# Kernel tuning notes

Hardware: AMD Instinct MI355X
Metric: run time of the kernel (lower is better)

Reference implementation:

```python
import jax, jax.numpy as jnp
import numpy as np

B = 8192
D_S, D_W, D_P, D_E, D_C, D_Z = 1024, 1024, 512, 1024, 512, 512
H_P = 2 * D_P          # particle hidden_dim default
RANK = D_W // 4        # low-rank A factor
EPS = 1e-5             # torch LayerNorm default eps


def _ln(x, g, b):
    m = jnp.mean(x, axis=-1, keepdims=True)
    v = jnp.var(x, axis=-1, keepdims=True)
    return (x - m) * jax.lax.rsqrt(v + EPS) * g + b


def setup_inputs() -> dict:
    key = jax.random.key(0)
    ks = iter(jax.random.split(key, 48))
    def randn(shape, scale=1.0):
        return jax.random.normal(next(ks), shape, dtype=jnp.float32) * scale
    def lin(dout, din):  # torch Linear: W [out,in], b [out]
        s = 1.0 / np.sqrt(din)
        return randn((dout, din), s), randn((dout,), s)
    inp = {}
    inp["s_prev"] = randn((B, D_S))
    inp["w_prev"] = randn((B, D_W))
    inp["p_prev"] = randn((B, D_P))
    inp["e_t"] = randn((B, D_E))
    inp["c_t"] = randn((B, D_C))
    d_in = D_S + D_E + D_C
    # fusion_net: Linear -> LN -> ReLU -> Linear
    inp["fw1"], inp["fb1"] = lin(2 * D_Z, d_in)
    inp["fln_g"] = jnp.ones((2 * D_Z,), jnp.float32)
    inp["fln_b"] = jnp.zeros((2 * D_Z,), jnp.float32)
    inp["fw2"], inp["fb2"] = lin(D_Z, 2 * D_Z)
    # wave subsystem
    inp["A_diag"] = jnp.zeros((D_W,), jnp.float32)
    inp["A_U"] = randn((D_W, RANK), 0.01)
    inp["A_V"] = randn((D_W, RANK), 0.01)
    inp["amod_w"], inp["amod_b"] = lin(D_W, D_C)
    inp["bnet_w"], inp["bnet_b"] = lin(D_W, D_C + D_Z)
    # particle subsystem phi
    inp["pw1"], inp["pb1"] = lin(H_P, D_P + D_Z + D_C)
    inp["pln_g"] = jnp.ones((H_P,), jnp.float32)
    inp["pln_b"] = jnp.zeros((H_P,), jnp.float32)
    inp["pw2"], inp["pb2"] = lin(H_P // 2, H_P)
    inp["pw3"], inp["pb3"] = lin(D_P, H_P // 2)
    # gate + mixing projections + output norm
    inp["gw"], inp["gb"] = lin(D_S, d_in)
    inp["uw"] = randn((D_S, D_W), 1.0 / np.sqrt(D_W))
    inp["up"] = randn((D_S, D_P), 1.0 / np.sqrt(D_P))
    inp["oln_g"] = jnp.ones((D_S,), jnp.float32)
    inp["oln_b"] = jnp.zeros((D_S,), jnp.float32)
    return inp


def reference(s_prev, w_prev, p_prev, e_t, c_t,
              fw1, fb1, fln_g, fln_b, fw2, fb2,
              A_diag, A_U, A_V, amod_w, amod_b, bnet_w, bnet_b,
              pw1, pb1, pln_g, pln_b, pw2, pb2, pw3, pb3,
              gw, gb, uw, up, oln_g, oln_b):
    # fusion: z_t = Linear(ReLU(LN(Linear([s||e||c]))))
    fin = jnp.concatenate([s_prev, e_t, c_t], axis=-1)      # [B, d_s+d_e+d_c]
    h = jax.nn.relu(_ln(fin @ fw1.T + fb1, fln_g, fln_b))
    z_t = h @ fw2.T + fb2                                   # [B, d_z]
    # wave: A = (diag(tanh(A_diag)*0.9) + A_U A_V^T) * mod[None,:]
    # so (A w)[b,i] = sum_j A_base[i,j] * (mod*w)[b,j] -> (mod*w) @ A_base^T
    A_base = jnp.diag(jnp.tanh(A_diag) * 0.9) + A_U @ A_V.T  # [d_w, d_w]
    mod = jnp.tanh(c_t @ amod_w.T + amod_b)                  # [B, d_w]
    w_linear = (mod * w_prev) @ A_base.T
    b_in = jnp.concatenate([c_t, z_t], axis=-1)
    w_t = w_linear + b_in @ bnet_w.T + bnet_b                # [B, d_w]
    # particle: p_t = p_prev + tanh(MLP([p||z||c]))
    pin = jnp.concatenate([p_prev, z_t, c_t], axis=-1)
    h1 = jax.nn.relu(_ln(pin @ pw1.T + pb1, pln_g, pln_b))
    h2 = jax.nn.relu(h1 @ pw2.T + pb2)
    p_t = p_prev + jnp.tanh(h2 @ pw3.T + pb3)                # [B, d_p]
    # gated mixing
    g_t = jax.nn.sigmoid(fin @ gw.T + gb)                    # [B, d_s]
    s_t = s_prev + g_t * (p_t @ up.T) + (1.0 - g_t) * (w_t @ uw.T)
    s_t = _ln(s_t, oln_g, oln_b)
    return (s_t, w_t, p_t)
```

## Files before the change

### kernel.cpp

```cpp
#include <hip/hip_runtime.h>
#include <math.h>

typedef unsigned short u16;
typedef __attribute__((ext_vector_type(8))) short short8;
typedef __attribute__((ext_vector_type(4))) float f32x4;

#define AS1C(p) ((const __attribute__((address_space(1))) void*)(p))
#define AS3(p)  ((__attribute__((address_space(3))) void*)(p))

static __device__ __forceinline__ float b2f(u16 h) {
    union { unsigned u; float f; } c; c.u = ((unsigned)h) << 16; return c.f;
}
static __device__ __forceinline__ u16 f2b(float f) {
    union { float f; unsigned u; } c; c.f = f;
    unsigned r = c.u + 0x7FFFu + ((c.u >> 16) & 1u);
    return (u16)(r >> 16);
}

#define EP_NONE     0
#define EP_RELU     1
#define EP_SIGMOID  2
#define EP_TANH_MUL 3
#define EP_TANH_ADD 4
#define EP_DIAG     5

struct GDesc {
    const u16* A;
    const u16* W;
    const float* bias;
    const float* auxf;
    u16* outb;
    float* outf;
    int lda, ldd, N, K, ep, nbm;
};

struct GArgs { GDesc d0, d1, d2; int s1, s2; };

__global__ __launch_bounds__(512, 2)
void gemm_8p(GArgs ga)
{
    __shared__ __align__(16) u16 LDS[65536];

    const int bid = (int)blockIdx.x;
    GDesc dd = (bid < ga.s1) ? ga.d0 : ((bid < ga.s2) ? ga.d1 : ga.d2);
    const int b = bid - ((bid < ga.s1) ? 0 : ((bid < ga.s2) ? ga.s1 : ga.s2));

    const int tid  = threadIdx.x;
    const int lane = tid & 63;
    const int wid  = tid >> 6;
    const int wr   = wid >> 2;
    const int wc   = wid & 3;

    const int bm = b % dd.nbm;
    const int bn = b / dd.nbm;
    const int lda = dd.lda, K = dd.K, N = dd.N, ldd = dd.ldd;
    const int nkt = K >> 6;

    const int srow  = tid >> 3;
    const int sslot = tid & 7;
    const int sgcol = (sslot ^ (srow & 7)) * 8;
    const u16* Ag = dd.A + (size_t)(bm * 256 + srow) * lda + sgcol;
    const u16* Wg = dd.W + (size_t)(bn * 256 + srow) * K + sgcol;
    const int ldst = tid * 8;

    f32x4 acc[8][4];
#pragma unroll
    for (int m = 0; m < 8; ++m)
#pragma unroll
        for (int n = 0; n < 4; ++n) acc[m][n] = (f32x4){0.f, 0.f, 0.f, 0.f};

#define STAGE_AH(bufi, kt, h)                                                    \
    {                                                                            \
        const int k0_ = (kt) << 6;                                               \
        u16* d_ = &LDS[(bufi) * 32768 + ldst];                                   \
        _Pragma("unroll")                                                        \
        for (int j = 2 * (h); j < 2 * (h) + 2; ++j)                              \
            __builtin_amdgcn_global_load_lds(AS1C(Ag + (size_t)(j * 64) * lda + k0_), \
                                             AS3(d_ + j * 4096), 16, 0, 0);      \
    }
#define STAGE_BH(bufi, kt, h)                                                    \
    {                                                                            \
        const int k0_ = (kt) << 6;                                               \
        u16* d_ = &LDS[(bufi) * 32768 + 16384 + ldst];                           \
        _Pragma("unroll")                                                        \
        for (int j = 2 * (h); j < 2 * (h) + 2; ++j)                              \
            __builtin_amdgcn_global_load_lds(AS1C(Wg + (size_t)(j * 64) * K + k0_),   \
                                             AS3(d_ + j * 4096), 16, 0, 0);      \
    }

#define VWAIT4()                                                                 \
    {                                                                            \
        __builtin_amdgcn_sched_barrier(0);                                       \
        asm volatile("s_waitcnt vmcnt(4)" ::: "memory");                         \
        __builtin_amdgcn_sched_barrier(0);                                       \
        __builtin_amdgcn_s_barrier();                                            \
        __builtin_amdgcn_sched_barrier(0);                                       \
    }

    const int swz  = (lane & 7) << 4;
    const int cnat = (lane >> 4) << 4;

    short8 AF0[4][2], AF1[4][2], BF[2][2];

#define LDA_SET(AF, mh, Al)                                                      \
    {                                                                            \
        const int rb_ = (mh) * 128 + wr * 64 + (lane & 15);                      \
        _Pragma("unroll")                                                        \
        for (int mm = 0; mm < 4; ++mm) {                                         \
            const u16* rp_ = (Al) + (rb_ + mm * 16) * 64;                        \
            _Pragma("unroll")                                                    \
            for (int ks = 0; ks < 2; ++ks)                                       \
                AF[mm][ks] = *(const short8*)(rp_ + ((((ks << 6) | cnat) ^ swz) >> 1)); \
        }                                                                        \
    }
#define LDB_SET(nh, Bl)                                                          \
    {                                                                            \
        const int rb_ = (nh) * 128 + wc * 32 + (lane & 15);                      \
        _Pragma("unroll")                                                        \
        for (int nn = 0; nn < 2; ++nn) {                                         \
            const u16* rp_ = (Bl) + (rb_ + nn * 16) * 64;                        \
            _Pragma("unroll")                                                    \
            for (int ks = 0; ks < 2; ++ks)                                       \
                BF[nn][ks] = *(const short8*)(rp_ + ((((ks << 6) | cnat) ^ swz) >> 1)); \
        }                                                                        \
    }
#define QMFMA(AF, mh, nh)                                                        \
    {                                                                            \
        __builtin_amdgcn_s_setprio(1);                                           \
        _Pragma("unroll")                                                        \
        for (int mm = 0; mm < 4; ++mm)                                           \
            _Pragma("unroll")                                                    \
            for (int nn = 0; nn < 2; ++nn)                                       \
                _Pragma("unroll")                                                \
                for (int ks = 0; ks < 2; ++ks)                                   \
                    acc[(mh) * 4 + mm][(nh) * 2 + nn] =                          \
                        __builtin_amdgcn_mfma_f32_16x16x32_bf16(                 \
                            AF[mm][ks], BF[nn][ks], acc[(mh) * 4 + mm][(nh) * 2 + nn], 0, 0, 0); \
        __builtin_amdgcn_s_setprio(0);                                           \
    }

    STAGE_AH(0, 0, 0);
    STAGE_BH(0, 0, 0);
    STAGE_AH(0, 0, 1);
    STAGE_BH(0, 0, 1);

    int buf = 0;
    for (int kt = 0; kt < nkt; ++kt) {
        const int ka = (kt + 1 < nkt) ? kt + 1 : nkt - 1;
        const u16* Al = &LDS[buf * 32768];
        const u16* Bl = Al + 16384;
        const int nb = buf ^ 1;

        VWAIT4();
        LDA_SET(AF0, 0, Al);
        LDB_SET(0, Bl);
        STAGE_AH(nb, ka, 0);
        QMFMA(AF0, 0, 0);

        VWAIT4();
        LDA_SET(AF1, 1, Al);
        STAGE_BH(nb, ka, 0);
        QMFMA(AF1, 1, 0);

        VWAIT4();
        LDB_SET(1, Bl);
        STAGE_AH(nb, ka, 1);
        QMFMA(AF1, 1, 1);

        __builtin_amdgcn_sched_barrier(0);
        STAGE_BH(nb, ka, 1);
        QMFMA(AF0, 0, 1);

        buf ^= 1;
    }

#undef STAGE_AH
#undef STAGE_BH
#undef VWAIT4
#undef LDA_SET
#undef LDB_SET
#undef QMFMA

    const int ep = dd.ep;
#pragma unroll
    for (int n = 0; n < 4; ++n) {
        const int C = bn * 256 + (n >> 1) * 128 + wc * 32 + (n & 1) * 16 + (lane & 15);
        const float bv = dd.bias ? dd.bias[C] : 0.f;
#pragma unroll
        for (int m = 0; m < 8; ++m) {
            const int R0 = bm * 256 + (m >> 2) * 128 + wr * 64 + (m & 3) * 16 + ((lane >> 4) << 2);
#pragma unroll
            for (int j = 0; j < 4; ++j) {
                const int R = R0 + j;
                float v = acc[m][n][j] + bv;
                if (ep == EP_RELU)          v = fmaxf(v, 0.f);
                else if (ep == EP_SIGMOID)  v = 1.f / (1.f + expf(-v));
                else if (ep == EP_TANH_MUL) v = tanhf(v) * dd.auxf[(size_t)R * N + C];
                else if (ep == EP_TANH_ADD) v = dd.auxf[(size_t)R * N + C] + tanhf(v);
                else if (ep == EP_DIAG)     { if (R == C) v += 0.9f * tanhf(dd.auxf[R]); }
                dd.outb[(size_t)R * ldd + C] = f2b(v);
                if (dd.outf) dd.outf[(size_t)R * N + C] = v;
            }
        }
    }
}

template<bool RELU>
__global__ __launch_bounds__(256)
void ln1024(u16* __restrict__ X, const float* __restrict__ gam, const float* __restrict__ bet)
{
    const int row = blockIdx.x;
    u16* xp = X + (size_t)row * 1024 + threadIdx.x * 4;
    u16 loc[4];
    *(uint2*)loc = *(const uint2*)xp;
    float x0 = b2f(loc[0]), x1 = b2f(loc[1]), x2 = b2f(loc[2]), x3 = b2f(loc[3]);
    float s = x0 + x1 + x2 + x3;
    float q = x0 * x0 + x1 * x1 + x2 * x2 + x3 * x3;
#pragma unroll
    for (int off = 32; off; off >>= 1) { s += __shfl_xor(s, off); q += __shfl_xor(q, off); }
    __shared__ float sm[8];
    const int wave = threadIdx.x >> 6, lane = threadIdx.x & 63;
    if (lane == 0) { sm[wave] = s; sm[4 + wave] = q; }
    __syncthreads();
    s = sm[0] + sm[1] + sm[2] + sm[3];
    q = sm[4] + sm[5] + sm[6] + sm[7];
    const float mean = s * (1.f / 1024.f);
    const float var  = q * (1.f / 1024.f) - mean * mean;
    const float inv  = rsqrtf(var + 1e-5f);
    const int cb = threadIdx.x * 4;
#pragma unroll
    for (int j = 0; j < 4; ++j) {
        float y = (b2f(loc[j]) - mean) * inv * gam[cb + j] + bet[cb + j];
        if (RELU) y = fmaxf(y, 0.f);
        loc[j] = f2b(y);
    }
    *(uint2*)xp = *(uint2*)loc;
}

__global__ __launch_bounds__(256)
void mix_ln(const float* __restrict__ sp, const u16* __restrict__ gt,
            const u16* __restrict__ pm, const u16* __restrict__ wm,
            const float* __restrict__ og, const float* __restrict__ ob,
            float* __restrict__ out)
{
    const int row = blockIdx.x;
    const size_t base = (size_t)row * 1024 + threadIdx.x * 4;
    float4 lsp = *(const float4*)(sp + base);
    u16 lg[4], lp[4], lw[4];
    *(uint2*)lg = *(const uint2*)(gt + base);
    *(uint2*)lp = *(const uint2*)(pm + base);
    *(uint2*)lw = *(const uint2*)(wm + base);
    float x[4];
    const float* lspp = (const float*)&lsp;
#pragma unroll
    for (int j = 0; j < 4; ++j) {
        float g = b2f(lg[j]);
        x[j] = lspp[j] + g * b2f(lp[j]) + (1.f - g) * b2f(lw[j]);
    }
    float s = x[0] + x[1] + x[2] + x[3];
    float q = x[0]*x[0] + x[1]*x[1] + x[2]*x[2] + x[3]*x[3];
#pragma unroll
    for (int off = 32; off; off >>= 1) { s += __shfl_xor(s, off); q += __shfl_xor(q, off); }
    __shared__ float sm[8];
    const int wave = threadIdx.x >> 6, lane = threadIdx.x & 63;
    if (lane == 0) { sm[wave] = s; sm[4 + wave] = q; }
    __syncthreads();
    s = sm[0] + sm[1] + sm[2] + sm[3];
    q = sm[4] + sm[5] + sm[6] + sm[7];
    const float mean = s * (1.f / 1024.f);
    const float var  = q * (1.f / 1024.f) - mean * mean;
    const float inv  = rsqrtf(var + 1e-5f);
    const int cb = threadIdx.x * 4;
    float4 o;
    float* op = (float*)&o;
#pragma unroll
    for (int j = 0; j < 4; ++j)
        op[j] = (x[j] - mean) * inv * og[cb + j] + ob[cb + j];
    *(float4*)(out + base) = o;
}

struct CDesc { const void* src; u16* dst; int srcCols8; int dstStride; int dstOff; unsigned end; int isbf16; };
struct CArgs { CDesc d[16]; unsigned total; };

__global__ __launch_bounds__(256)
void multi_copy(CArgs ca)
{
    const unsigned idx = blockIdx.x * 256 + threadIdx.x;
    if (idx >= ca.total) return;
    int i = 0; unsigned start = 0;
    while (idx >= ca.d[i].end) { start = ca.d[i].end; ++i; }
    const CDesc cd = ca.d[i];
    const unsigned local = idx - start;
    const int r = local / cd.srcCols8;
    const int c = local % cd.srcCols8;
    u16 o[8];
    if (cd.isbf16) {
        *(uint4*)o = *(const uint4*)((const u16*)cd.src + ((size_t)r * cd.srcCols8 + c) * 8);
    } else {
        const float* s = (const float*)cd.src + ((size_t)r * cd.srcCols8 + c) * 8;
        const float4 a = *(const float4*)s;
        const float4 bq = *(const float4*)(s + 4);
        const float* ap = (const float*)&a;
        const float* bp = (const float*)&bq;
#pragma unroll
        for (int j = 0; j < 4; ++j) { o[j] = f2b(ap[j]); o[4 + j] = f2b(bp[j]); }
    }
    *(uint4*)(cd.dst + (size_t)r * cd.dstStride + cd.dstOff + (size_t)c * 8) = *(uint4*)o;
}

extern "C" void kernel_launch(void* const* d_in, const int* in_sizes, int n_in,
                              void* d_out, int out_size, void* d_ws, size_t ws_size,
                              hipStream_t stream)
{
    const float* s_prev = (const float*)d_in[0];
    const float* w_prev = (const float*)d_in[1];
    const float* p_prev = (const float*)d_in[2];
    const float* e_t    = (const float*)d_in[3];
    const float* c_t    = (const float*)d_in[4];
    const float* fw1    = (const float*)d_in[5];
    const float* fb1    = (const float*)d_in[6];
    const float* fln_g  = (const float*)d_in[7];
    const float* fln_b  = (const float*)d_in[8];
    const float* fw2    = (const float*)d_in[9];
    const float* fb2    = (const float*)d_in[10];
    const float* A_diag = (const float*)d_in[11];
    const float* A_U    = (const float*)d_in[12];
    const float* A_V    = (const float*)d_in[13];
    const float* amod_w = (const float*)d_in[14];
    const float* amod_b = (const float*)d_in[15];
    const float* bnet_w = (const float*)d_in[16];
    const float* bnet_b = (const float*)d_in[17];
    const float* pw1    = (const float*)d_in[18];
    const float* pb1    = (const float*)d_in[19];
    const float* pln_g  = (const float*)d_in[20];
    const float* pln_b  = (const float*)d_in[21];
    const float* pw2    = (const float*)d_in[22];
    const float* pb2    = (const float*)d_in[23];
    const float* pw3    = (const float*)d_in[24];
    const float* pb3    = (const float*)d_in[25];
    const float* gw     = (const float*)d_in[26];
    const float* gb     = (const float*)d_in[27];
    const float* uw     = (const float*)d_in[28];
    const float* up     = (const float*)d_in[29];
    const float* oln_g  = (const float*)d_in[30];
    const float* oln_b  = (const float*)d_in[31];

    float* out_s = (float*)d_out;
    float* out_w = out_s + (size_t)8192 * 1024;
    float* out_p = out_w + (size_t)8192 * 1024;

    u16* ws = (u16*)d_ws;
    u16* FIN  = ws;
    u16* W_bf = ws + 12582912;
    u16* H    = ws + 20971520;
    u16* P_bf = H;
    u16* Z    = ws + 29360128;
    u16* G    = ws + 33554432;
    u16* ACAT = ws + 41943040;
    u16* PM   = ACAT;
    u16* WM   = ACAT + 8388608;
    u16* WCAT = ws + 58720256;
    u16* wb   = ws + 60817408;
    u16* fw1b  = wb;
    u16* gwb   = wb + 2621440;
    u16* fw2b  = wb + 5242880;
    u16* amodb = wb + 5767168;
    u16* pw1b  = wb + 6291456;
    u16* pw2b  = wb + 7864320;
    u16* pw3b  = wb + 8388608;
    u16* uwb   = wb + 8650752;
    u16* upb   = wb + 9699328;
    u16* AUb   = wb + 10223616;
    u16* AVb   = wb + 10485760;

    const dim3 blk(256);
    const dim3 blk512(512);

    {
        CArgs ca; unsigned cum = 0; int nd = 0;
        auto push = [&](const void* src, u16* dst, int cols8, int stride, int off,
                        int rows, int isbf) {
            cum += (unsigned)rows * cols8;
            ca.d[nd++] = CDesc{src, dst, cols8, stride, off, cum, isbf};
        };
        push(fw1,    fw1b,  320, 2560, 0,    1024, 0);
        push(gw,     gwb,   320, 2560, 0,    1024, 0);
        push(fw2,    fw2b,  128, 1024, 0,    512,  0);
        push(amod_w, amodb, 64,  512,  0,    1024, 0);
        push(pw1,    pw1b,  192, 1536, 0,    1024, 0);
        push(pw2,    pw2b,  128, 1024, 0,    512,  0);
        push(pw3,    pw3b,  64,  512,  0,    512,  0);
        push(uw,     uwb,   128, 1024, 0,    1024, 0);
        push(up,     upb,   64,  512,  0,    1024, 0);
        push(A_U,    AUb,   32,  256,  0,    1024, 0);
        push(A_V,    AVb,   32,  256,  0,    1024, 0);
        push(s_prev, FIN,   128, 2560, 0,    8192, 0);
        push(e_t,    FIN,   128, 2560, 1024, 8192, 0);
        push(c_t,    FIN,   64,  2560, 2048, 8192, 0);
        push(c_t,    ACAT,  64,  2048, 1024, 8192, 0);
        push(bnet_w, WCAT,  128, 2048, 1024, 1024, 0);
        ca.total = cum;
        multi_copy<<<dim3((cum + 255) / 256), blk, 0, stream>>>(ca);
    }

    {
        GArgs ga;
        ga.d0 = GDesc{FIN, fw1b, fb1, nullptr, H, nullptr, 2560, 1024, 1024, 2560, EP_NONE,    32};
        ga.d1 = GDesc{FIN, gwb,  gb,  nullptr, G, nullptr, 2560, 1024, 1024, 2560, EP_SIGMOID, 32};
        ga.d2 = ga.d1; ga.s1 = 128; ga.s2 = 256;
        gemm_8p<<<dim3(256), blk512, 0, stream>>>(ga);
    }
    ln1024<true><<<8192, blk, 0, stream>>>(H, fln_g, fln_b);

    {
        GArgs ga;
        ga.d0 = GDesc{H,          fw2b,  fb2,     nullptr, Z,    nullptr, 1024, 512,  512,  1024, EP_NONE,     32};
        ga.d1 = GDesc{FIN + 2048, amodb, amod_b,  w_prev,  ACAT, nullptr, 2560, 2048, 1024, 512,  EP_TANH_MUL, 32};
        ga.d2 = GDesc{AUb,        AVb,   nullptr, A_diag,  WCAT, nullptr, 256,  2048, 1024, 256,  EP_DIAG,     4};
        ga.s1 = 64; ga.s2 = 192;
        gemm_8p<<<dim3(208), blk512, 0, stream>>>(ga);
    }

    {
        CArgs ca; unsigned cum = 0; int nd = 0;
        auto push = [&](const void* src, u16* dst, int cols8, int stride, int off,
                        int rows, int isbf) {
            cum += (unsigned)rows * cols8;
            ca.d[nd++] = CDesc{src, dst, cols8, stride, off, cum, isbf};
        };
        push(p_prev, FIN,  64, 1536, 0,    8192, 0);
        push(Z,      FIN,  64, 1536, 512,  8192, 1);
        push(c_t,    FIN,  64, 1536, 1024, 8192, 0);
        push(Z,      ACAT, 64, 2048, 1536, 8192, 1);
        ca.total = cum;
        multi_copy<<<dim3((cum + 255) / 256), blk, 0, stream>>>(ca);
    }

    {
        GArgs ga;
        ga.d0 = GDesc{ACAT, WCAT, bnet_b, nullptr, W_bf, out_w,   2048, 1024, 1024, 2048, EP_NONE, 32};
        ga.d1 = GDesc{FIN,  pw1b, pb1,    nullptr, H,    nullptr, 1536, 1024, 1024, 1536, EP_NONE, 32};
        ga.d2 = ga.d1; ga.s1 = 128; ga.s2 = 256;
        gemm_8p<<<dim3(256), blk512, 0, stream>>>(ga);
    }
    ln1024<true><<<8192, blk, 0, stream>>>(H, pln_g, pln_b);

    {
        GArgs ga;
        ga.d0 = GDesc{H,    pw2b, pb2,     nullptr, Z,  nullptr, 1024, 512,  512,  1024, EP_RELU, 32};
        ga.d1 = GDesc{W_bf, uwb,  nullptr, nullptr, WM, nullptr, 1024, 1024, 1024, 1024, EP_NONE, 32};
        ga.d2 = ga.d1; ga.s1 = 64; ga.s2 = 192;
        gemm_8p<<<dim3(192), blk512, 0, stream>>>(ga);
    }

    {
        GArgs ga;
        ga.d0 = GDesc{Z, pw3b, pb3, p_prev, P_bf, out_p, 512, 512, 512, 512, EP_TANH_ADD, 32};
        ga.d1 = ga.d0; ga.d2 = ga.d0; ga.s1 = 64; ga.s2 = 64;
        gemm_8p<<<dim3(64), blk512, 0, stream>>>(ga);
    }

    {
        GArgs ga;
        ga.d0 = GDesc{P_bf, upb, nullptr, nullptr, PM, nullptr, 512, 1024, 1024, 512, EP_NONE, 32};
        ga.d1 = ga.d0; ga.d2 = ga.d0; ga.s1 = 128; ga.s2 = 128;
        gemm_8p<<<dim3(128), blk512, 0, stream>>>(ga);
    }

    mix_ln<<<8192, blk, 0, stream>>>(s_prev, G, PM, WM, oln_g, oln_b, out_s);
}
```

Before: 529.5 us.

## Software-pipeline LDS fragment reads one quadrant ahead of MFMA in GEMM main loop

Restructures the GEMM k-loop so the LDS fragment reads for the next quadrant (and the next k-tile's first A/B fragments) are issued right after each MFMA quadrant. This lets LDS latency overlap with tensor-core work instead of stalling before each quadrant. The loop is unrolled by two to hard-code the double-buffer pointers, and LDS addresses are precomputed once to cut per-iteration address arithmetic. In exchange it needs extra fragment registers (separate B0/B1 sets), which raises register pressure at two waves per SIMD. The barrier and waitcnt ordering also becomes more delicate, and it assumes an even number of k-tiles.

```diff
diff --git a/kernel.cpp b/kernel.cpp
--- a/kernel.cpp
+++ b/kernel.cpp
@@ -37,7 +37,7 @@
 struct GArgs { GDesc d0, d1, d2; int s1, s2; };
 
 __global__ __launch_bounds__(512, 2)
-void gemm_8p(GArgs ga)
+void gemm_v2(GArgs ga)
 {
     __shared__ __align__(16) u16 LDS[65536];
 
@@ -69,26 +69,56 @@
 #pragma unroll
         for (int n = 0; n < 4; ++n) acc[m][n] = (f32x4){0.f, 0.f, 0.f, 0.f};
 
-#define STAGE_AH(bufi, kt, h)                                                    \
-    {                                                                            \
-        const int k0_ = (kt) << 6;                                               \
+    const int swz  = (lane & 7) << 4;
+    const int cnat = (lane >> 4) << 4;
+    const int aRow = (wr * 64 + (lane & 15)) * 64;
+    const int bRow = (wc * 32 + (lane & 15)) * 64;
+    const u16* pA00 = LDS + aRow + ((cnat ^ swz) >> 1);
+    const u16* pA10 = LDS + aRow + ((((64) | cnat) ^ swz) >> 1);
+    const u16* pA01 = pA00 + 32768;
+    const u16* pA11 = pA10 + 32768;
+    const u16* pB00 = LDS + 16384 + bRow + ((cnat ^ swz) >> 1);
+    const u16* pB10 = LDS + 16384 + bRow + ((((64) | cnat) ^ swz) >> 1);
+    const u16* pB01 = pB00 + 32768;
+    const u16* pB11 = pB10 + 32768;
+
+    short8 A0f[4][2], A1f[4][2], B0f[2][2], B1f[2][2];
+
+#define READ_A(AF, PK0, PK1, MHOFF)                                              \
+    {                                                                            \
+        _Pragma("unroll")                                                        \
+        for (int mm = 0; mm < 4; ++mm) {                                         \
+            AF[mm][0] = *(const short8*)((PK0) + (MHOFF) + mm * 1024);           \
+            AF[mm][1] = *(const short8*)((PK1) + (MHOFF) + mm * 1024);           \
+        }                                                                        \
+    }
+#define READ_B(BF, PK0, PK1, NHOFF)                                              \
+    {                                                                            \
+        _Pragma("unroll")                                                        \
+        for (int nn = 0; nn < 2; ++nn) {                                         \
+            BF[nn][0] = *(const short8*)((PK0) + (NHOFF) + nn * 1024);           \
+            BF[nn][1] = *(const short8*)((PK1) + (NHOFF) + nn * 1024);           \
+        }                                                                        \
+    }
+
+#define STAGE_A(bufi, k0_, h)                                                    \
+    {                                                                            \
         u16* d_ = &LDS[(bufi) * 32768 + ldst];                                   \
         _Pragma("unroll")                                                        \
         for (int j = 2 * (h); j < 2 * (h) + 2; ++j)                              \
-            __builtin_amdgcn_global_load_lds(AS1C(Ag + (size_t)(j * 64) * lda + k0_), \
+            __builtin_amdgcn_global_load_lds(AS1C(Ag + (size_t)(j * 64) * lda + (k0_)), \
                                              AS3(d_ + j * 4096), 16, 0, 0);      \
     }
-#define STAGE_BH(bufi, kt, h)                                                    \
-    {                                                                            \
-        const int k0_ = (kt) << 6;                                               \
+#define STAGE_B(bufi, k0_, h)                                                    \
+    {                                                                            \
         u16* d_ = &LDS[(bufi) * 32768 + 16384 + ldst];                           \
         _Pragma("unroll")                                                        \
         for (int j = 2 * (h); j < 2 * (h) + 2; ++j)                              \
-            __builtin_amdgcn_global_load_lds(AS1C(Wg + (size_t)(j * 64) * K + k0_),   \
+            __builtin_amdgcn_global_load_lds(AS1C(Wg + (size_t)(j * 64) * K + (k0_)),   \
                                              AS3(d_ + j * 4096), 16, 0, 0);      \
     }
 
-#define VWAIT4()                                                                 \
+#define VW4()                                                                    \
     {                                                                            \
         __builtin_amdgcn_sched_barrier(0);                                       \
         asm volatile("s_waitcnt vmcnt(4)" ::: "memory");                         \
@@ -97,34 +127,7 @@
         __builtin_amdgcn_sched_barrier(0);                                       \
     }
 
-    const int swz  = (lane & 7) << 4;
-    const int cnat = (lane >> 4) << 4;
-
-    short8 AF0[4][2], AF1[4][2], BF[2][2];
-
-#define LDA_SET(AF, mh, Al)                                                      \
-    {                                                                            \
-        const int rb_ = (mh) * 128 + wr * 64 + (lane & 15);                      \
-        _Pragma("unroll")                                                        \
-        for (int mm = 0; mm < 4; ++mm) {                                         \
-            const u16* rp_ = (Al) + (rb_ + mm * 16) * 64;                        \
-            _Pragma("unroll")                                                    \
-            for (int ks = 0; ks < 2; ++ks)                                       \
-                AF[mm][ks] = *(const short8*)(rp_ + ((((ks << 6) | cnat) ^ swz) >> 1)); \
-        }                                                                        \
-    }
-#define LDB_SET(nh, Bl)                                                          \
-    {                                                                            \
-        const int rb_ = (nh) * 128 + wc * 32 + (lane & 15);                      \
-        _Pragma("unroll")                                                        \
-        for (int nn = 0; nn < 2; ++nn) {                                         \
-            const u16* rp_ = (Bl) + (rb_ + nn * 16) * 64;                        \
-            _Pragma("unroll")                                                    \
-            for (int ks = 0; ks < 2; ++ks)                                       \
-                BF[nn][ks] = *(const short8*)(rp_ + ((((ks << 6) | cnat) ^ swz) >> 1)); \
-        }                                                                        \
-    }
-#define QMFMA(AF, mh, nh)                                                        \
+#define QMFMA(AF, BF, mh, nh)                                                    \
     {                                                                            \
         __builtin_amdgcn_s_setprio(1);                                           \
         _Pragma("unroll")                                                        \
@@ -139,47 +142,59 @@
         __builtin_amdgcn_s_setprio(0);                                           \
     }
 
-    STAGE_AH(0, 0, 0);
-    STAGE_BH(0, 0, 0);
-    STAGE_AH(0, 0, 1);
-    STAGE_BH(0, 0, 1);
-
-    int buf = 0;
-    for (int kt = 0; kt < nkt; ++kt) {
-        const int ka = (kt + 1 < nkt) ? kt + 1 : nkt - 1;
-        const u16* Al = &LDS[buf * 32768];
-        const u16* Bl = Al + 16384;
-        const int nb = buf ^ 1;
-
-        VWAIT4();
-        LDA_SET(AF0, 0, Al);
-        LDB_SET(0, Bl);
-        STAGE_AH(nb, ka, 0);
-        QMFMA(AF0, 0, 0);
-
-        VWAIT4();
-        LDA_SET(AF1, 1, Al);
-        STAGE_BH(nb, ka, 0);
-        QMFMA(AF1, 1, 0);
-
-        VWAIT4();
-        LDB_SET(1, Bl);
-        STAGE_AH(nb, ka, 1);
-        QMFMA(AF1, 1, 1);
-
-        __builtin_amdgcn_sched_barrier(0);
-        STAGE_BH(nb, ka, 1);
-        QMFMA(AF0, 0, 1);
-
-        buf ^= 1;
-    }
-
-#undef STAGE_AH
-#undef STAGE_BH
-#undef VWAIT4
-#undef LDA_SET
-#undef LDB_SET
+#define TILE(NBUF, CA0, CA1, CBp0, CBp1, NA0, NA1, NBp0, NBp1, ktv)              \
+    {                                                                            \
+        const int ka_ = ((ktv) + 1 < nkt) ? (ktv) + 1 : nkt - 1;                 \
+        const int k0n = ka_ << 6;                                                \
+            \
+        STAGE_A(NBUF, k0n, 0);                                                   \
+        VW4();                                                                   \
+        QMFMA(A0f, B0f, 0, 0);                                                   \
+        READ_B(B1f, CBp0, CBp1, 8192);                                           \
+            \
+        STAGE_B(NBUF, k0n, 0);                                                   \
+        VW4();                                                                   \
+        QMFMA(A0f, B1f, 0, 1);                                                   \
+        READ_A(A1f, CA0, CA1, 8192);                                             \
+         \
+        STAGE_B(NBUF, k0n, 1);                                                   \
+        VW4();                                                                   \
+        QMFMA(A1f, B1f, 1, 1);                                                   \
+        READ_A(A0f, NA0, NA1, 0);                                                \
+         \
+        STAGE_A(NBUF, k0n, 1);                                                   \
+        VW4();                                                                   \
+        QMFMA(A1f, B0f, 1, 0);                                                   \
+        READ_B(B0f, NBp0, NBp1, 0);                                              \
+    }
+
+    STAGE_A(0, 0, 0);
+    __builtin_amdgcn_sched_barrier(0);
+    STAGE_B(0, 0, 0);
+    __builtin_amdgcn_sched_barrier(0);
+    STAGE_B(0, 0, 1);
+    __builtin_amdgcn_sched_barrier(0);
+    STAGE_A(0, 0, 1);
+    __builtin_amdgcn_sched_barrier(0);
+    asm volatile("s_waitcnt vmcnt(4)" ::: "memory");
+    __builtin_amdgcn_sched_barrier(0);
+    __builtin_amdgcn_s_barrier();
+    __builtin_amdgcn_sched_barrier(0);
+    READ_A(A0f, pA00, pA10, 0);
+    READ_B(B0f, pB00, pB10, 0);
+
+    for (int kt = 0; kt < nkt; kt += 2) {
+        TILE(1, pA00, pA10, pB00, pB10, pA01, pA11, pB01, pB11, kt);
+        TILE(0, pA01, pA11, pB01, pB11, pA00, pA10, pB00, pB10, kt + 1);
+    }
+
+#undef READ_A
+#undef READ_B
+#undef STAGE_A
+#undef STAGE_B
+#undef VW4
 #undef QMFMA
+#undef TILE
 
     const int ep = dd.ep;
 #pragma unroll
@@ -408,7 +423,7 @@
         ga.d0 = GDesc{FIN, fw1b, fb1, nullptr, H, nullptr, 2560, 1024, 1024, 2560, EP_NONE,    32};
         ga.d1 = GDesc{FIN, gwb,  gb,  nullptr, G, nullptr, 2560, 1024, 1024, 2560, EP_SIGMOID, 32};
         ga.d2 = ga.d1; ga.s1 = 128; ga.s2 = 256;
-        gemm_8p<<<dim3(256), blk512, 0, stream>>>(ga);
+        gemm_v2<<<dim3(256), blk512, 0, stream>>>(ga);
     }
     ln1024<true><<<8192, blk, 0, stream>>>(H, fln_g, fln_b);
 
@@ -418,7 +433,7 @@
         ga.d1 = GDesc{FIN + 2048, amodb, amod_b,  w_prev,  ACAT, nullptr, 2560, 2048, 1024, 512,  EP_TANH_MUL, 32};
         ga.d2 = GDesc{AUb,        AVb,   nullptr, A_diag,  WCAT, nullptr, 256,  2048, 1024, 256,  EP_DIAG,     4};
         ga.s1 = 64; ga.s2 = 192;
-        gemm_8p<<<dim3(208), blk512, 0, stream>>>(ga);
+        gemm_v2<<<dim3(208), blk512, 0, stream>>>(ga);
     }
 
     {
@@ -441,7 +456,7 @@
         ga.d0 = GDesc{ACAT, WCAT, bnet_b, nullptr, W_bf, out_w,   2048, 1024, 1024, 2048, EP_NONE, 32};
         ga.d1 = GDesc{FIN,  pw1b, pb1,    nullptr, H,    nullptr, 1536, 1024, 1024, 1536, EP_NONE, 32};
         ga.d2 = ga.d1; ga.s1 = 128; ga.s2 = 256;
-        gemm_8p<<<dim3(256), blk512, 0, stream>>>(ga);
+        gemm_v2<<<dim3(256), blk512, 0, stream>>>(ga);
     }
     ln1024<true><<<8192, blk, 0, stream>>>(H, pln_g, pln_b);
 
@@ -450,21 +465,21 @@
         ga.d0 = GDesc{H,    pw2b, pb2,     nullptr, Z,  nullptr, 1024, 512,  512,  1024, EP_RELU, 32};
         ga.d1 = GDesc{W_bf, uwb,  nullptr, nullptr, WM, nullptr, 1024, 1024, 1024, 1024, EP_NONE, 32};
         ga.d2 = ga.d1; ga.s1 = 64; ga.s2 = 192;
-        gemm_8p<<<dim3(192), blk512, 0, stream>>>(ga);
+        gemm_v2<<<dim3(192), blk512, 0, stream>>>(ga);
     }
 
     {
         GArgs ga;
         ga.d0 = GDesc{Z, pw3b, pb3, p_prev, P_bf, out_p, 512, 512, 512, 512, EP_TANH_ADD, 32};
         ga.d1 = ga.d0; ga.d2 = ga.d0; ga.s1 = 64; ga.s2 = 64;
-        gemm_8p<<<dim3(64), blk512, 0, stream>>>(ga);
+        gemm_v2<<<dim3(64), blk512, 0, stream>>>(ga);
     }
 
     {
         GArgs ga;
         ga.d0 = GDesc{P_bf, upb, nullptr, nullptr, PM, nullptr, 512, 1024, 1024, 512, EP_NONE, 32};
         ga.d1 = ga.d0; ga.d2 = ga.d0; ga.s1 = 128; ga.s2 = 128;
-        gemm_8p<<<dim3(128), blk512, 0, stream>>>(ga);
+        gemm_v2<<<dim3(128), blk512, 0, stream>>>(ga);
     }
 
     mix_ln<<<8192, blk, 0, stream>>>(s_prev, G, PM, WM, oln_g, oln_b, out_s);
```

Result: no change. 519.3 us (-1.9%).
